# Kernel tuning notes

Hardware: AMD Instinct MI355X
Metric: run time of the kernel (lower is better)

Reference implementation:

```python
import jax, jax.numpy as jnp
import numpy as np

N = 4096
NFEAT = 512
NHID = 64
NHEADS = 8
NCLASS = 41
ALPHA = 0.2          # LeakyReLU negative slope
NEG = -9e15          # mask fill value from the torch code
EDGE_P = 0.004       # ~16 avg degree


def _xavier_uniform(key, shape, gain=1.414):
    fan_in, fan_out = shape[-2], shape[-1]
    limit = gain * np.sqrt(6.0 / (fan_in + fan_out))
    return jax.random.uniform(key, shape, jnp.float32, -limit, limit)


def setup_inputs() -> dict:
    key = jax.random.key(0)
    ks = jax.random.split(key, 6)
    x = jax.random.normal(ks[0], (N, NFEAT), jnp.float32)
    # sparse random graph, densified (module calls adj.to_dense()); add self-loops
    adj = (jax.random.uniform(ks[1], (N, N)) < EDGE_P).astype(jnp.float32)
    adj = jnp.maximum(adj, jnp.eye(N, dtype=jnp.float32))
    # 8 attention heads (nfeat -> nhid), stacked
    W_heads = _xavier_uniform(ks[2], (NHEADS, NFEAT, NHID))
    a_heads = _xavier_uniform(ks[3], (NHEADS, 2 * NHID, 1))
    # output attention layer (nhid*nheads -> nclass)
    W_out = _xavier_uniform(ks[4], (NHEADS * NHID, NCLASS))
    a_out = _xavier_uniform(ks[5], (2 * NCLASS, 1))
    return {"x": x, "adj": adj, "W_heads": W_heads, "a_heads": a_heads,
            "W_out": W_out, "a_out": a_out}


def _leaky_relu(e):
    return jnp.where(e > 0, e, ALPHA * e)


def reference(x, adj, W_heads, a_heads, W_out, a_out):
    # inference mode: all dropout layers are identity (training=False)
    mask = adj > 0                                   # [N, N]
    # ---- multi-head GAT layer (concat=True, ELU inside layer) ----
    Wh = jnp.einsum('nf,hfd->hnd', x, W_heads)       # [H, N, D]
    a1 = a_heads[:, :NHID, 0]                        # [H, D]
    a2 = a_heads[:, NHID:, 0]                        # [H, D]
    s1 = jnp.einsum('hnd,hd->hn', Wh, a1)            # [H, N]
    s2 = jnp.einsum('hnd,hd->hn', Wh, a2)            # [H, N]
    e = _leaky_relu(s1[:, :, None] + s2[:, None, :])  # [H, N, N]
    att = jax.nn.softmax(jnp.where(mask[None], e, NEG), axis=-1)
    h = jax.nn.elu(jnp.einsum('hnm,hmd->hnd', att, Wh))   # [H, N, D]
    h = jnp.transpose(h, (1, 0, 2)).reshape(N, NHEADS * NHID)  # concat heads
    # ---- output GAT layer (concat=False) + ELU (with_relu=True) ----
    Wh2 = h @ W_out                                  # [N, C]
    e2 = _leaky_relu(Wh2 @ a_out[:NCLASS] + (Wh2 @ a_out[NCLASS:]).T)  # [N, N]
    att2 = jax.nn.softmax(jnp.where(mask, e2, NEG), axis=-1)
    out = jax.nn.elu(att2 @ Wh2)                     # [N, C]
    # mode='t', multi_label falsy -> log_softmax
    return jax.nn.log_softmax(out, axis=1)
```

## Files before the change

### kernel.cpp

```cpp
#include <hip/hip_runtime.h>
#include <hip/hip_bf16.h>
#include <math.h>


#define N 4096
#define NFEAT 512
#define NHID 64
#define NHEADS 8
#define NCLASS 41
#define NCPAD 48
#define ALPHA 0.2f
#define ELLW 64

using short8  = __attribute__((ext_vector_type(8))) short;
using floatx4 = __attribute__((ext_vector_type(4))) float;

__device__ __forceinline__ float wred_max(float v) {
#pragma unroll
  for (int o = 32; o; o >>= 1) v = fmaxf(v, __shfl_xor(v, o, 64));
  return v;
}
__device__ __forceinline__ float wred_sum(float v) {
#pragma unroll
  for (int o = 32; o; o >>= 1) v += __shfl_xor(v, o, 64);
  return v;
}

__device__ __forceinline__ void split_bf16(float v, short& hi, short& lo) {
  __hip_bfloat16 hb = __float2bfloat16(v);
  float hf = __bfloat162float(hb);
  __hip_bfloat16 lb = __float2bfloat16(v - hf);
  hi = *reinterpret_cast<short*>(&hb);
  lo = *reinterpret_cast<short*>(&lb);
}

__global__ __launch_bounds__(256) void setup(const float* __restrict__ x,
                                             const float* __restrict__ W,
                                             const float* __restrict__ W_out,
                                             const float* __restrict__ adj,
                                             short* __restrict__ Xhi,
                                             short* __restrict__ Xlo,
                                             short* __restrict__ Wthi,
                                             short* __restrict__ Wtlo,
                                             short* __restrict__ WOhi,
                                             short* __restrict__ WOlo,
                                             int* __restrict__ cols,
                                             int* __restrict__ cnts) {
  if (blockIdx.x >= 2208) {
    __shared__ int c;
    const int row = blockIdx.x - 2208;
    if (threadIdx.x == 0) c = 0;
    __syncthreads();
    const float4* arow = (const float4*)(adj + (size_t)row * N);
    for (int j4 = threadIdx.x; j4 < N / 4; j4 += 256) {
      float4 v = arow[j4];
      if (v.x > 0.f) { int p = atomicAdd(&c, 1); if (p < ELLW) cols[row * ELLW + p] = j4 * 4 + 0; }
      if (v.y > 0.f) { int p = atomicAdd(&c, 1); if (p < ELLW) cols[row * ELLW + p] = j4 * 4 + 1; }
      if (v.z > 0.f) { int p = atomicAdd(&c, 1); if (p < ELLW) cols[row * ELLW + p] = j4 * 4 + 2; }
      if (v.w > 0.f) { int p = atomicAdd(&c, 1); if (p < ELLW) cols[row * ELLW + p] = j4 * 4 + 3; }
    }
    __syncthreads();
    if (threadIdx.x == 0) cnts[row] = min(c, ELLW);
  } else if (blockIdx.x < 2048) {
    const int t = blockIdx.x * 256 + threadIdx.x;
    const float4 v = ((const float4*)x)[t];
    short h0, l0, h1, l1, h2, l2, h3, l3;
    split_bf16(v.x, h0, l0);
    split_bf16(v.y, h1, l1);
    split_bf16(v.z, h2, l2);
    split_bf16(v.w, h3, l3);
    ((short4*)Xhi)[t] = make_short4(h0, h1, h2, h3);
    ((short4*)Xlo)[t] = make_short4(l0, l1, l2, l3);
  } else if (blockIdx.x < 2112) {
    __shared__ float tile[64][65];
    const int idx = blockIdx.x - 2048;
    const int h = idx >> 3, k0 = (idx & 7) * 64;
    const int t = threadIdx.x;
#pragma unroll
    for (int i = 0; i < 4; i++) {
      const int g = t + 256 * i;
      const int r = g >> 4, c4 = g & 15;
      const float4 v = *(const float4*)&W[(size_t)h * 32768 + (size_t)(k0 + r) * 64 + c4 * 4];
      tile[r][c4 * 4 + 0] = v.x;
      tile[r][c4 * 4 + 1] = v.y;
      tile[r][c4 * 4 + 2] = v.z;
      tile[r][c4 * 4 + 3] = v.w;
    }
    __syncthreads();
#pragma unroll
    for (int i = 0; i < 2; i++) {
      const int g = t + 256 * i;
      const int d = g >> 3, kg = (g & 7) * 8;
      short8 hv, lv;
#pragma unroll
      for (int j = 0; j < 8; j++) {
        short hh, ll;
        split_bf16(tile[kg + j][d], hh, ll);
        hv[j] = hh;
        lv[j] = ll;
      }
      const size_t dst = (size_t)h * 32768 + (size_t)d * 512 + k0 + kg;
      *(short8*)&Wthi[dst] = hv;
      *(short8*)&Wtlo[dst] = lv;
    }
  } else {
    const int t = (blockIdx.x - 2112) * 256 + threadIdx.x;
    const int c = t >> 9, k = t & 511;
    float v = (c < NCLASS) ? W_out[(size_t)k * NCLASS + c] : 0.f;
    short hi, lo;
    split_bf16(v, hi, lo);
    WOhi[c * 512 + k] = hi;
    WOlo[c * 512 + k] = lo;
  }
}

__global__ __launch_bounds__(128) void wh_gemm_mfma(
    const short* __restrict__ Xhi, const short* __restrict__ Xlo,
    const short* __restrict__ Wthi, const short* __restrict__ Wtlo,
    const float* __restrict__ a_heads,
    float* __restrict__ Wh, float* __restrict__ s1, float* __restrict__ s2) {
  __shared__ __align__(16) short Ahi[64 * 72];
  __shared__ __align__(16) short Alo[64 * 72];
  __shared__ __align__(16) short Bhi[64 * 72];
  __shared__ __align__(16) short Blo[64 * 72];
  const int id = blockIdx.x;
  const int h = (id >> 3) & 7;
  const int tile = (id & 7) + ((id >> 6) << 3);
  const int n0 = tile * 64;
  const int tid = threadIdx.x;
  const int w = tid >> 6, L = tid & 63;

  floatx4 acc[2][4];
#pragma unroll
  for (int rt = 0; rt < 2; rt++)
#pragma unroll
    for (int f = 0; f < 4; f++) acc[rt][f] = (floatx4){0.f, 0.f, 0.f, 0.f};

  for (int k0 = 0; k0 < NFEAT; k0 += 64) {
    __syncthreads();
#pragma unroll
    for (int i = 0; i < 4; i++) {
      const int g = tid + 128 * i;
      const int row = g >> 3, kg = (g & 7) * 8;
      const size_t asrc = (size_t)(n0 + row) * NFEAT + k0 + kg;
      *(uint4*)&Ahi[row * 72 + kg] = *(const uint4*)&Xhi[asrc];
      *(uint4*)&Alo[row * 72 + kg] = *(const uint4*)&Xlo[asrc];
      const size_t bsrc = (size_t)h * 32768 + (size_t)row * 512 + k0 + kg;
      *(uint4*)&Bhi[row * 72 + kg] = *(const uint4*)&Wthi[bsrc];
      *(uint4*)&Blo[row * 72 + kg] = *(const uint4*)&Wtlo[bsrc];
    }
    __syncthreads();
#pragma unroll
    for (int ks = 0; ks < 2; ks++) {
      const int koff = ks * 32 + (L >> 4) * 8;
      const int abase = (w * 32 + (L & 15)) * 72 + koff;
      short8 ahi0 = *(const short8*)&Ahi[abase];
      short8 alo0 = *(const short8*)&Alo[abase];
      short8 ahi1 = *(const short8*)&Ahi[abase + 16 * 72];
      short8 alo1 = *(const short8*)&Alo[abase + 16 * 72];
#pragma unroll
      for (int f = 0; f < 4; f++) {
        short8 bhi = *(const short8*)&Bhi[(f * 16 + (L & 15)) * 72 + koff];
        short8 blo = *(const short8*)&Blo[(f * 16 + (L & 15)) * 72 + koff];
        acc[0][f] = __builtin_amdgcn_mfma_f32_16x16x32_bf16(ahi0, bhi, acc[0][f], 0, 0, 0);
        acc[0][f] = __builtin_amdgcn_mfma_f32_16x16x32_bf16(ahi0, blo, acc[0][f], 0, 0, 0);
        acc[0][f] = __builtin_amdgcn_mfma_f32_16x16x32_bf16(alo0, bhi, acc[0][f], 0, 0, 0);
        acc[1][f] = __builtin_amdgcn_mfma_f32_16x16x32_bf16(ahi1, bhi, acc[1][f], 0, 0, 0);
        acc[1][f] = __builtin_amdgcn_mfma_f32_16x16x32_bf16(ahi1, blo, acc[1][f], 0, 0, 0);
        acc[1][f] = __builtin_amdgcn_mfma_f32_16x16x32_bf16(alo1, bhi, acc[1][f], 0, 0, 0);
      }
    }
  }

  const int q = L >> 4, c16 = L & 15;
  float a1v[4], a2v[4];
#pragma unroll
  for (int f = 0; f < 4; f++) {
    a1v[f] = a_heads[h * 128 + f * 16 + c16];
    a2v[f] = a_heads[h * 128 + 64 + f * 16 + c16];
  }
#pragma unroll
  for (int rt = 0; rt < 2; rt++) {
    float p1[4] = {0.f, 0.f, 0.f, 0.f}, p2[4] = {0.f, 0.f, 0.f, 0.f};
#pragma unroll
    for (int f = 0; f < 4; f++)
#pragma unroll
      for (int r = 0; r < 4; r++) {
        const float vv = acc[rt][f][r];
        const int row = n0 + w * 32 + rt * 16 + q * 4 + r;
        Wh[((size_t)(h << 12) + row) * NHID + f * 16 + c16] = vv;
        p1[r] += vv * a1v[f];
        p2[r] += vv * a2v[f];
      }
#pragma unroll
    for (int r = 0; r < 4; r++)
#pragma unroll
      for (int o = 1; o < 16; o <<= 1) {
        p1[r] += __shfl_xor(p1[r], o, 64);
        p2[r] += __shfl_xor(p2[r], o, 64);
      }
    if (c16 == 0) {
      const int row = n0 + w * 32 + rt * 16 + q * 4;
#pragma unroll
      for (int r = 0; r < 4; r++) {
        s1[(h << 12) + row + r] = p1[r];
        s2[(h << 12) + row + r] = p2[r];
      }
    }
  }
}

__global__ __launch_bounds__(256) void att1_kernel(
    const float* __restrict__ Wh, const float* __restrict__ s1,
    const float* __restrict__ s2, const int* __restrict__ cols,
    const int* __restrict__ cnts, short* __restrict__ Hhi,
    short* __restrict__ Hlo) {
  __shared__ float pj[4][68];
  __shared__ int jj[4][68];
  const int w = threadIdx.x >> 6, lane = threadIdx.x & 63;
  const int pair = blockIdx.x * 4 + w;
  const int h = pair >> 12, i = pair & (N - 1);
  const int cnt = cnts[i];
  const float s1i = s1[(h << 12) + i];
  const float* s2h = s2 + (h << 12);
  float e0 = -1e30f;
  int j0 = 0;
  if (lane < cnt) {
    j0 = cols[i * ELLW + lane];
    float t = s1i + s2h[j0];
    e0 = t > 0.f ? t : ALPHA * t;
  }
  const float m = wred_max(e0);
  float p = (lane < cnt) ? expf(e0 - m) : 0.f;
  const float S = wred_sum(p);
  p *= 1.f / S;
  pj[w][lane] = p;
  jj[w][lane] = (lane < cnt) ? j0 : 0;
  if (lane < 4) { pj[w][64 + lane] = 0.f; jj[w][64 + lane] = 0; }
  __syncthreads();
  const int grp = lane >> 4, c4 = lane & 15;
  const float* Whh = Wh + (((size_t)h << 12)) * NHID;
  float4 acc = make_float4(0.f, 0.f, 0.f, 0.f);
  for (int t0 = 0; t0 < cnt; t0 += 4) {
    const float pt = pj[w][t0 + grp];
    const int jt = jj[w][t0 + grp];
    const float4 v = *(const float4*)&Whh[(size_t)jt * NHID + c4 * 4];
    acc.x += pt * v.x; acc.y += pt * v.y; acc.z += pt * v.z; acc.w += pt * v.w;
  }
#pragma unroll
  for (int off = 16; off <= 32; off <<= 1) {
    acc.x += __shfl_xor(acc.x, off, 64);
    acc.y += __shfl_xor(acc.y, off, 64);
    acc.z += __shfl_xor(acc.z, off, 64);
    acc.w += __shfl_xor(acc.w, off, 64);
  }
  if (grp == 0) {
    const float o0 = acc.x > 0.f ? acc.x : expf(acc.x) - 1.f;
    const float o1 = acc.y > 0.f ? acc.y : expf(acc.y) - 1.f;
    const float o2 = acc.z > 0.f ? acc.z : expf(acc.z) - 1.f;
    const float o3 = acc.w > 0.f ? acc.w : expf(acc.w) - 1.f;
    short h0, l0, h1, l1, h2, l2, h3, l3;
    split_bf16(o0, h0, l0);
    split_bf16(o1, h1, l1);
    split_bf16(o2, h2, l2);
    split_bf16(o3, h3, l3);
    const size_t base = (size_t)i * 512 + h * 64 + c4 * 4;
    *(short4*)&Hhi[base] = make_short4(h0, h1, h2, h3);
    *(short4*)&Hlo[base] = make_short4(l0, l1, l2, l3);
  }
}

__global__ __launch_bounds__(256) void gemm2_mfma(
    const short* __restrict__ Hhi, const short* __restrict__ Hlo,
    const short* __restrict__ WOhi, const short* __restrict__ WOlo,
    const float* __restrict__ a_out,
    float* __restrict__ Wh2, float* __restrict__ s1b, float* __restrict__ s2b) {
  __shared__ float red[3][64][12];
  const int n0 = blockIdx.x * 16;
  const int tid = threadIdx.x;
  const int w = tid >> 6, L = tid & 63;
  const int r15 = L & 15;

  floatx4 acc[3];
#pragma unroll
  for (int f = 0; f < 3; f++) acc[f] = (floatx4){0.f, 0.f, 0.f, 0.f};

#pragma unroll
  for (int ks = 0; ks < 4; ks++) {
    const int koff = w * 128 + ks * 32 + (L >> 4) * 8;
    const short8 ahi = *(const short8*)&Hhi[(size_t)(n0 + r15) * 512 + koff];
    const short8 alo = *(const short8*)&Hlo[(size_t)(n0 + r15) * 512 + koff];
#pragma unroll
    for (int f = 0; f < 3; f++) {
      const short8 bhi = *(const short8*)&WOhi[(size_t)(f * 16 + r15) * 512 + koff];
      const short8 blo = *(const short8*)&WOlo[(size_t)(f * 16 + r15) * 512 + koff];
      acc[f] = __builtin_amdgcn_mfma_f32_16x16x32_bf16(ahi, bhi, acc[f], 0, 0, 0);
      acc[f] = __builtin_amdgcn_mfma_f32_16x16x32_bf16(ahi, blo, acc[f], 0, 0, 0);
      acc[f] = __builtin_amdgcn_mfma_f32_16x16x32_bf16(alo, bhi, acc[f], 0, 0, 0);
    }
  }

  if (w) {
#pragma unroll
    for (int f = 0; f < 3; f++)
#pragma unroll
      for (int r = 0; r < 4; r++) red[w - 1][L][f * 4 + r] = acc[f][r];
  }
  __syncthreads();
  if (w == 0) {
    const int q = L >> 4, c16 = r15;
    float a1v[3], a2v[3];
#pragma unroll
    for (int f = 0; f < 3; f++) {
      const int col = f * 16 + c16;
      a1v[f] = (col < NCLASS) ? a_out[col] : 0.f;
      a2v[f] = (col < NCLASS) ? a_out[NCLASS + col] : 0.f;
    }
    float p1[4] = {0.f, 0.f, 0.f, 0.f}, p2[4] = {0.f, 0.f, 0.f, 0.f};
#pragma unroll
    for (int f = 0; f < 3; f++)
#pragma unroll
      for (int r = 0; r < 4; r++) {
        const float vv = acc[f][r] + red[0][L][f * 4 + r] + red[1][L][f * 4 + r] +
                         red[2][L][f * 4 + r];
        const int col = f * 16 + c16;
        const int row = n0 + q * 4 + r;
        if (col < NCLASS) Wh2[(size_t)row * NCLASS + col] = vv;
        p1[r] += vv * a1v[f];
        p2[r] += vv * a2v[f];
      }
#pragma unroll
    for (int r = 0; r < 4; r++)
#pragma unroll
      for (int o = 1; o < 16; o <<= 1) {
        p1[r] += __shfl_xor(p1[r], o, 64);
        p2[r] += __shfl_xor(p2[r], o, 64);
      }
    if (c16 == 0) {
      const int row = n0 + q * 4;
#pragma unroll
      for (int r = 0; r < 4; r++) {
        s1b[row + r] = p1[r];
        s2b[row + r] = p2[r];
      }
    }
  }
}

__global__ __launch_bounds__(256) void att2_kernel(const float* __restrict__ Wh2,
                                                   const float* __restrict__ s1b,
                                                   const float* __restrict__ s2b,
                                                   const int* __restrict__ cols,
                                                   const int* __restrict__ cnts,
                                                   float* __restrict__ out) {
  __shared__ float pj[4][64];
  __shared__ int jj[4][64];
  const int w = threadIdx.x >> 6, lane = threadIdx.x & 63;
  const int i = blockIdx.x * 4 + w;
  const int cnt = cnts[i];
  const float s1i = s1b[i];
  float e0 = -1e30f;
  int j0 = 0;
  if (lane < cnt) {
    j0 = cols[i * ELLW + lane];
    float t = s1i + s2b[j0];
    e0 = t > 0.f ? t : ALPHA * t;
  }
  const float m = wred_max(e0);
  float p = (lane < cnt) ? expf(e0 - m) : 0.f;
  const float S = wred_sum(p);
  p *= 1.f / S;
  pj[w][lane] = p;
  jj[w][lane] = (lane < cnt) ? j0 : 0;
  __syncthreads();
  float acc = 0.f;
  for (int t = 0; t < cnt; t++) {
    const float pt = pj[w][t];
    const int jt = jj[w][t];
    if (lane < NCLASS) acc += pt * Wh2[(size_t)jt * NCLASS + lane];
  }
  const float o = acc > 0.f ? acc : expf(acc) - 1.f;
  const float vv = (lane < NCLASS) ? o : -1e30f;
  const float mm = wred_max(vv);
  const float ex = (lane < NCLASS) ? expf(o - mm) : 0.f;
  const float SS = wred_sum(ex);
  if (lane < NCLASS) out[(size_t)i * NCLASS + lane] = o - mm - logf(SS);
}

extern "C" void kernel_launch(void* const* d_in, const int* in_sizes, int n_in,
                              void* d_out, int out_size, void* d_ws, size_t ws_size,
                              hipStream_t stream) {
  const float* x       = (const float*)d_in[0];
  const float* adj     = (const float*)d_in[1];
  const float* W_heads = (const float*)d_in[2];
  const float* a_heads = (const float*)d_in[3];
  const float* W_out   = (const float*)d_in[4];
  const float* a_out   = (const float*)d_in[5];
  float* out = (float*)d_out;

  float* ws   = (float*)d_ws;
  float* Wh   = ws;
  float* s1   = Wh + (size_t)NHEADS * N * NHID;
  float* s2   = s1 + NHEADS * N;
  float* Wh2  = s2 + NHEADS * N;
  float* s1b  = Wh2 + (size_t)N * NCLASS;
  float* s2b  = s1b + N;
  int* cnts   = (int*)(s2b + N);
  int* cols   = cnts + N;
  short* Xhi  = (short*)(cols + N * ELLW);
  short* Xlo  = Xhi + (size_t)N * NFEAT;
  short* Wthi = Xlo + (size_t)N * NFEAT;
  short* Wtlo = Wthi + (size_t)NHEADS * NHID * NFEAT;
  short* WOhi = Wtlo + (size_t)NHEADS * NHID * NFEAT;
  short* WOlo = WOhi + (size_t)NCPAD * 512;
  short* Hhi  = WOlo + (size_t)NCPAD * 512;
  short* Hlo  = Hhi + (size_t)N * NFEAT;

  hipLaunchKernelGGL(setup, dim3(6304), dim3(256), 0, stream,
                     x, W_heads, W_out, adj, Xhi, Xlo, Wthi, Wtlo, WOhi, WOlo, cols, cnts);
  hipLaunchKernelGGL(wh_gemm_mfma, dim3(NHEADS * N / 64), dim3(128), 0, stream,
                     Xhi, Xlo, Wthi, Wtlo, a_heads, Wh, s1, s2);
  hipLaunchKernelGGL(att1_kernel, dim3(NHEADS * N / 4), dim3(256), 0, stream,
                     Wh, s1, s2, cols, cnts, Hhi, Hlo);
  hipLaunchKernelGGL(gemm2_mfma, dim3(N / 16), dim3(256), 0, stream,
                     Hhi, Hlo, WOhi, WOlo, a_out, Wh2, s1b, s2b);
  hipLaunchKernelGGL(att2_kernel, dim3(N / 4), dim3(256), 0, stream,
                     Wh2, s1b, s2b, cols, cnts, out);
}
```

Before: 159.6 us.

## Move adjacency ELL build into GEMM kernel and drop LDS staging

The adjacency-to-ELL scan moves out of the setup kernel and into extra blocks of the Wh GEMM kernel, so the 64 MB adj read overlaps with the MFMA GEMM rather than being serialized ahead of it. The GEMM also drops its shared-memory tiles and barriers and loads bf16 hi/lo fragments straight from global memory into MFMA operands. This trades LDS traffic and syncs for more redundant global/L2 loads of the weight fragments.

```diff
diff --git a/kernel.cpp b/kernel.cpp
--- a/kernel.cpp
+++ b/kernel.cpp
@@ -37,31 +37,13 @@
 __global__ __launch_bounds__(256) void setup(const float* __restrict__ x,
                                              const float* __restrict__ W,
                                              const float* __restrict__ W_out,
-                                             const float* __restrict__ adj,
                                              short* __restrict__ Xhi,
                                              short* __restrict__ Xlo,
                                              short* __restrict__ Wthi,
                                              short* __restrict__ Wtlo,
                                              short* __restrict__ WOhi,
-                                             short* __restrict__ WOlo,
-                                             int* __restrict__ cols,
-                                             int* __restrict__ cnts) {
-  if (blockIdx.x >= 2208) {
-    __shared__ int c;
-    const int row = blockIdx.x - 2208;
-    if (threadIdx.x == 0) c = 0;
-    __syncthreads();
-    const float4* arow = (const float4*)(adj + (size_t)row * N);
-    for (int j4 = threadIdx.x; j4 < N / 4; j4 += 256) {
-      float4 v = arow[j4];
-      if (v.x > 0.f) { int p = atomicAdd(&c, 1); if (p < ELLW) cols[row * ELLW + p] = j4 * 4 + 0; }
-      if (v.y > 0.f) { int p = atomicAdd(&c, 1); if (p < ELLW) cols[row * ELLW + p] = j4 * 4 + 1; }
-      if (v.z > 0.f) { int p = atomicAdd(&c, 1); if (p < ELLW) cols[row * ELLW + p] = j4 * 4 + 2; }
-      if (v.w > 0.f) { int p = atomicAdd(&c, 1); if (p < ELLW) cols[row * ELLW + p] = j4 * 4 + 3; }
-    }
-    __syncthreads();
-    if (threadIdx.x == 0) cnts[row] = min(c, ELLW);
-  } else if (blockIdx.x < 2048) {
+                                             short* __restrict__ WOlo) {
+  if (blockIdx.x < 2048) {
     const int t = blockIdx.x * 256 + threadIdx.x;
     const float4 v = ((const float4*)x)[t];
     short h0, l0, h1, l1, h2, l2, h3, l3;
@@ -114,21 +96,35 @@
   }
 }
 
-__global__ __launch_bounds__(128) void wh_gemm_mfma(
+__global__ __launch_bounds__(128) void wh_gemm_ell(
     const short* __restrict__ Xhi, const short* __restrict__ Xlo,
     const short* __restrict__ Wthi, const short* __restrict__ Wtlo,
-    const float* __restrict__ a_heads,
-    float* __restrict__ Wh, float* __restrict__ s1, float* __restrict__ s2) {
-  __shared__ __align__(16) short Ahi[64 * 72];
-  __shared__ __align__(16) short Alo[64 * 72];
-  __shared__ __align__(16) short Bhi[64 * 72];
-  __shared__ __align__(16) short Blo[64 * 72];
+    const float* __restrict__ a_heads, const float* __restrict__ adj,
+    float* __restrict__ Wh, float* __restrict__ s1, float* __restrict__ s2,
+    int* __restrict__ cols, int* __restrict__ cnts) {
+  __shared__ int c;
   const int id = blockIdx.x;
+  if (id >= 512) {
+    const int row = id - 512;
+    if (threadIdx.x == 0) c = 0;
+    __syncthreads();
+    const float4* arow = (const float4*)(adj + (size_t)row * N);
+    for (int j4 = threadIdx.x; j4 < N / 4; j4 += 128) {
+      float4 v = arow[j4];
+      if (v.x > 0.f) { int p = atomicAdd(&c, 1); if (p < ELLW) cols[row * ELLW + p] = j4 * 4 + 0; }
+      if (v.y > 0.f) { int p = atomicAdd(&c, 1); if (p < ELLW) cols[row * ELLW + p] = j4 * 4 + 1; }
+      if (v.z > 0.f) { int p = atomicAdd(&c, 1); if (p < ELLW) cols[row * ELLW + p] = j4 * 4 + 2; }
+      if (v.w > 0.f) { int p = atomicAdd(&c, 1); if (p < ELLW) cols[row * ELLW + p] = j4 * 4 + 3; }
+    }
+    __syncthreads();
+    if (threadIdx.x == 0) cnts[row] = min(c, ELLW);
+    return;
+  }
   const int h = (id >> 3) & 7;
   const int tile = (id & 7) + ((id >> 6) << 3);
   const int n0 = tile * 64;
-  const int tid = threadIdx.x;
-  const int w = tid >> 6, L = tid & 63;
+  const int w = threadIdx.x >> 6, L = threadIdx.x & 63;
+  const int q = L >> 4, r15 = L & 15;
 
   floatx4 acc[2][4];
 #pragma unroll
@@ -136,43 +132,32 @@
 #pragma unroll
     for (int f = 0; f < 4; f++) acc[rt][f] = (floatx4){0.f, 0.f, 0.f, 0.f};
 
-  for (int k0 = 0; k0 < NFEAT; k0 += 64) {
-    __syncthreads();
-#pragma unroll
-    for (int i = 0; i < 4; i++) {
-      const int g = tid + 128 * i;
-      const int row = g >> 3, kg = (g & 7) * 8;
-      const size_t asrc = (size_t)(n0 + row) * NFEAT + k0 + kg;
-      *(uint4*)&Ahi[row * 72 + kg] = *(const uint4*)&Xhi[asrc];
-      *(uint4*)&Alo[row * 72 + kg] = *(const uint4*)&Xlo[asrc];
-      const size_t bsrc = (size_t)h * 32768 + (size_t)row * 512 + k0 + kg;
-      *(uint4*)&Bhi[row * 72 + kg] = *(const uint4*)&Wthi[bsrc];
-      *(uint4*)&Blo[row * 72 + kg] = *(const uint4*)&Wtlo[bsrc];
-    }
-    __syncthreads();
-#pragma unroll
-    for (int ks = 0; ks < 2; ks++) {
-      const int koff = ks * 32 + (L >> 4) * 8;
-      const int abase = (w * 32 + (L & 15)) * 72 + koff;
-      short8 ahi0 = *(const short8*)&Ahi[abase];
-      short8 alo0 = *(const short8*)&Alo[abase];
-      short8 ahi1 = *(const short8*)&Ahi[abase + 16 * 72];
-      short8 alo1 = *(const short8*)&Alo[abase + 16 * 72];
-#pragma unroll
-      for (int f = 0; f < 4; f++) {
-        short8 bhi = *(const short8*)&Bhi[(f * 16 + (L & 15)) * 72 + koff];
-        short8 blo = *(const short8*)&Blo[(f * 16 + (L & 15)) * 72 + koff];
-        acc[0][f] = __builtin_amdgcn_mfma_f32_16x16x32_bf16(ahi0, bhi, acc[0][f], 0, 0, 0);
-        acc[0][f] = __builtin_amdgcn_mfma_f32_16x16x32_bf16(ahi0, blo, acc[0][f], 0, 0, 0);
-        acc[0][f] = __builtin_amdgcn_mfma_f32_16x16x32_bf16(alo0, bhi, acc[0][f], 0, 0, 0);
-        acc[1][f] = __builtin_amdgcn_mfma_f32_16x16x32_bf16(ahi1, bhi, acc[1][f], 0, 0, 0);
-        acc[1][f] = __builtin_amdgcn_mfma_f32_16x16x32_bf16(ahi1, blo, acc[1][f], 0, 0, 0);
-        acc[1][f] = __builtin_amdgcn_mfma_f32_16x16x32_bf16(alo1, bhi, acc[1][f], 0, 0, 0);
-      }
-    }
-  }
-
-  const int q = L >> 4, c16 = L & 15;
+  const short* Ah = Xhi + (size_t)(n0 + w * 32 + r15) * NFEAT;
+  const short* Al = Xlo + (size_t)(n0 + w * 32 + r15) * NFEAT;
+  const short* Bh = Wthi + (size_t)h * 32768;
+  const short* Bl = Wtlo + (size_t)h * 32768;
+
+#pragma unroll 4
+  for (int ks = 0; ks < 16; ks++) {
+    const int ko = ks * 32 + q * 8;
+    const short8 ahi0 = *(const short8*)&Ah[ko];
+    const short8 alo0 = *(const short8*)&Al[ko];
+    const short8 ahi1 = *(const short8*)&Ah[16 * NFEAT + ko];
+    const short8 alo1 = *(const short8*)&Al[16 * NFEAT + ko];
+#pragma unroll
+    for (int f = 0; f < 4; f++) {
+      const short8 bhi = *(const short8*)&Bh[(size_t)(f * 16 + r15) * 512 + ko];
+      const short8 blo = *(const short8*)&Bl[(size_t)(f * 16 + r15) * 512 + ko];
+      acc[0][f] = __builtin_amdgcn_mfma_f32_16x16x32_bf16(ahi0, bhi, acc[0][f], 0, 0, 0);
+      acc[0][f] = __builtin_amdgcn_mfma_f32_16x16x32_bf16(ahi0, blo, acc[0][f], 0, 0, 0);
+      acc[0][f] = __builtin_amdgcn_mfma_f32_16x16x32_bf16(alo0, bhi, acc[0][f], 0, 0, 0);
+      acc[1][f] = __builtin_amdgcn_mfma_f32_16x16x32_bf16(ahi1, bhi, acc[1][f], 0, 0, 0);
+      acc[1][f] = __builtin_amdgcn_mfma_f32_16x16x32_bf16(ahi1, blo, acc[1][f], 0, 0, 0);
+      acc[1][f] = __builtin_amdgcn_mfma_f32_16x16x32_bf16(alo1, bhi, acc[1][f], 0, 0, 0);
+    }
+  }
+
+  const int c16 = r15;
   float a1v[4], a2v[4];
 #pragma unroll
   for (int f = 0; f < 4; f++) {
@@ -416,10 +401,10 @@
   short* Hhi  = WOlo + (size_t)NCPAD * 512;
   short* Hlo  = Hhi + (size_t)N * NFEAT;
 
-  hipLaunchKernelGGL(setup, dim3(6304), dim3(256), 0, stream,
-                     x, W_heads, W_out, adj, Xhi, Xlo, Wthi, Wtlo, WOhi, WOlo, cols, cnts);
-  hipLaunchKernelGGL(wh_gemm_mfma, dim3(NHEADS * N / 64), dim3(128), 0, stream,
-                     Xhi, Xlo, Wthi, Wtlo, a_heads, Wh, s1, s2);
+  hipLaunchKernelGGL(setup, dim3(2208), dim3(256), 0, stream,
+                     x, W_heads, W_out, Xhi, Xlo, Wthi, Wtlo, WOhi, WOlo);
+  hipLaunchKernelGGL(wh_gemm_ell, dim3(512 + N), dim3(128), 0, stream,
+                     Xhi, Xlo, Wthi, Wtlo, a_heads, adj, Wh, s1, s2, cols, cnts);
   hipLaunchKernelGGL(att1_kernel, dim3(NHEADS * N / 4), dim3(256), 0, stream,
                      Wh, s1, s2, cols, cnts, Hhi, Hlo);
   hipLaunchKernelGGL(gemm2_mfma, dim3(N / 16), dim3(256), 0, stream,
```

Result: slower. 172.2 us (+7.9%).
